# Kernel optimization log

Measured on AMD Instinct MI355X. Metric: run time of the kernel, lower is better.

Reference implementation:

```python
import jax, jax.numpy as jnp
import numpy as np

TWO_PI = 2.0 * 3.14159  # matches the torch source constant exactly
N_RINGS = 5
N_ORIENT = 8


def setup_inputs() -> dict:
    key = jax.random.key(0)
    k1, k2, k3 = jax.random.split(key, 3)
    B, N, CIN, COUT = 4, 32768, 32, 32
    features = jax.random.normal(k1, (B, N, CIN), dtype=jnp.float32)
    # radial in [0,1), angular in [0, 2*pi)
    coords01 = jax.random.uniform(k2, (B, N, 2), dtype=jnp.float32)
    geodesic_coords = coords01 * jnp.array([1.0, TWO_PI], dtype=jnp.float32)
    filters = jax.random.normal(k3, (N_RINGS, N_ORIENT, CIN, COUT), dtype=jnp.float32) * 0.01
    bias = jnp.zeros((COUT,), dtype=jnp.float32)
    return {"features": features, "geodesic_coords": geodesic_coords,
            "filters": filters, "bias": bias}


def reference(features, geodesic_coords, filters, bias):
    radial = geodesic_coords[:, :, 0]
    angular = geodesic_coords[:, :, 1]
    # torch .long() truncates toward zero; values are non-negative so astype matches
    ring_idx = jnp.clip((radial * N_RINGS).astype(jnp.int32), 0, N_RINGS - 1)
    orient_idx = jnp.clip((angular * N_ORIENT / TWO_PI).astype(jnp.int32), 0, N_ORIENT - 1)
    # gather per-point filter matrix: (B, N, Cin, Cout)
    W = filters[ring_idx, orient_idx]
    out = jnp.einsum('bnc,bncd->bnd', features, W) + bias
    return out
```

## Files before the change

kernel.cpp:

```cpp
#include <hip/hip_runtime.h>


#define NBINS 40
#define THREADS 1024
#define PTS_BLK 512

typedef __attribute__((ext_vector_type(8))) short bf16x8;
typedef __attribute__((ext_vector_type(4))) float f32x4;

__device__ __forceinline__ unsigned short f2bf(float x) {
    unsigned u = __float_as_uint(x);
    u += 0x7FFFu + ((u >> 16) & 1u);
    return (unsigned short)(u >> 16);
}

__device__ __forceinline__ int bin_of(float2 rc) {
    const float TWO_PI_F = (float)(2.0 * 3.14159);
    int ri = (int)(rc.x * 5.0f);
    ri = min(max(ri, 0), 4);
    int oi = (int)((rc.y * 8.0f) / TWO_PI_F);
    oi = min(max(oi, 0), 7);
    return ri * 8 + oi;
}

__global__ __launch_bounds__(THREADS, 4)
void k_fused(const float* __restrict__ feat, const float2* __restrict__ coords,
             const float* __restrict__ filt, const float* __restrict__ bias,
             float* __restrict__ out) {
    __shared__ __align__(16) unsigned short Wl[NBINS * 2 * 64 * 8];
    __shared__ int wlist[16][32];

    const int tid  = threadIdx.x;
    const int lane = tid & 63;
    const int wave = tid >> 6;
    const int l15  = lane & 15;
    const int kg   = lane >> 4;
    const int pbase = blockIdx.x * PTS_BLK + wave * 32;

    for (int it = tid; it < NBINS * 128; it += THREADS) {
        const int il = it & 15, ik = (it >> 4) & 3, in = (it >> 6) & 1, ib = it >> 7;
        const float* src = filt + ib * 1024 + ik * 256 + in * 16 + il;
        bf16x8 w;
        #pragma unroll
        for (int j = 0; j < 8; ++j) w[j] = (short)f2bf(src[j * 32]);
        *reinterpret_cast<bf16x8*>(&Wl[it * 8]) = w;
    }

    const int myb = bin_of(coords[pbase + (lane & 31)]);
    bf16x8 af[2];
    #pragma unroll
    for (int m = 0; m < 2; ++m) {
        const float* fp = feat + (size_t)(pbase + m * 16 + l15) * 32 + kg * 8;
        const float4 v0 = *reinterpret_cast<const float4*>(fp);
        const float4 v1 = *reinterpret_cast<const float4*>(fp + 4);
        bf16x8 a;
        a[0] = (short)f2bf(v0.x); a[1] = (short)f2bf(v0.y);
        a[2] = (short)f2bf(v0.z); a[3] = (short)f2bf(v0.w);
        a[4] = (short)f2bf(v1.x); a[5] = (short)f2bf(v1.y);
        a[6] = (short)f2bf(v1.z); a[7] = (short)f2bf(v1.w);
        af[m] = a;
    }
    const int bm0 = __shfl(myb, l15);
    const int bm1 = __shfl(myb, 16 + l15);

    int cnt = 0;
    unsigned long long rem = __ballot(1);
    while (rem) {
        const int src = (int)__ffsll((long long)rem) - 1;
        const int bb  = __shfl(myb, src);
        rem &= ~__ballot(myb == bb);
        if (lane == 0) wlist[wave][cnt] = bb;
        ++cnt;
    }

    __syncthreads();

    f32x4 acc[2][2];
    {
        const float bv0 = bias[l15];
        const float bv1 = bias[16 + l15];
        #pragma unroll
        for (int m = 0; m < 2; ++m) {
            acc[m][0] = (f32x4){bv0, bv0, bv0, bv0};
            acc[m][1] = (f32x4){bv1, bv1, bv1, bv1};
        }
    }

    int bb = wlist[wave][0];
    bf16x8 B0 = *reinterpret_cast<const bf16x8*>(&Wl[((bb * 2 + 0) * 64 + lane) * 8]);
    bf16x8 B1 = *reinterpret_cast<const bf16x8*>(&Wl[((bb * 2 + 1) * 64 + lane) * 8]);
    for (int i = 0; i < cnt; ++i) {
        const int nx  = (i + 1 < cnt) ? i + 1 : i;
        const int bbn = wlist[wave][nx];
        const bf16x8 N0 = *reinterpret_cast<const bf16x8*>(&Wl[((bbn * 2 + 0) * 64 + lane) * 8]);
        const bf16x8 N1 = *reinterpret_cast<const bf16x8*>(&Wl[((bbn * 2 + 1) * 64 + lane) * 8]);
        bf16x8 a0 = af[0]; if (bm0 != bb) a0 = (bf16x8)0;
        bf16x8 a1 = af[1]; if (bm1 != bb) a1 = (bf16x8)0;
        acc[0][0] = __builtin_amdgcn_mfma_f32_16x16x32_bf16(a0, B0, acc[0][0], 0, 0, 0);
        acc[0][1] = __builtin_amdgcn_mfma_f32_16x16x32_bf16(a0, B1, acc[0][1], 0, 0, 0);
        acc[1][0] = __builtin_amdgcn_mfma_f32_16x16x32_bf16(a1, B0, acc[1][0], 0, 0, 0);
        acc[1][1] = __builtin_amdgcn_mfma_f32_16x16x32_bf16(a1, B1, acc[1][1], 0, 0, 0);
        bb = bbn; B0 = N0; B1 = N1;
    }

    #pragma unroll
    for (int m = 0; m < 2; ++m)
        #pragma unroll
        for (int r = 0; r < 4; ++r) {
            const size_t o = (size_t)(pbase + m * 16 + kg * 4 + r) * 32;
            out[o + l15]      = acc[m][0][r];
            out[o + 16 + l15] = acc[m][1][r];
        }
}

extern "C" void kernel_launch(void* const* d_in, const int* in_sizes, int n_in,
                              void* d_out, int out_size, void* d_ws, size_t ws_size,
                              hipStream_t stream) {
    const float*  feat   = (const float*)d_in[0];
    const float2* coords = (const float2*)d_in[1];
    const float*  filt   = (const float*)d_in[2];
    const float*  bias   = (const float*)d_in[3];
    float* out = (float*)d_out;

    const int npts = in_sizes[0] / 32;
    k_fused<<<npts / PTS_BLK, THREADS, 0, stream>>>(feat, coords, filt, bias, out);
}
```

Before: 80.87 us.

## Sort block points by bin and load filter fragments directly from global

Each block now builds a histogram of its 512 points' bins in shared memory, computes prefix offsets, and ranks points so that each wave processes points grouped by filter bin. This cuts the number of distinct bins per wave and so the number of masked MFMA passes. The per-block conversion of all 40 filters into LDS is removed, and each wave instead gathers and converts its needed filter fragments straight from global memory with strided scalar loads. The cost is extra syncs and atomics, gathered feature and output rows that are no longer contiguous, and uncoalesced filter loads on the critical path.

```diff
diff --git a/kernel.cpp b/kernel.cpp
--- a/kernel.cpp
+++ b/kernel.cpp
@@ -27,7 +27,10 @@
 void k_fused(const float* __restrict__ feat, const float2* __restrict__ coords,
              const float* __restrict__ filt, const float* __restrict__ bias,
              float* __restrict__ out) {
-    __shared__ __align__(16) unsigned short Wl[NBINS * 2 * 64 * 8];
+    __shared__ int hist[NBINS];
+    __shared__ int offs[NBINS];
+    __shared__ int bins[PTS_BLK];
+    __shared__ int rank[PTS_BLK];
     __shared__ int wlist[16][32];
 
     const int tid  = threadIdx.x;
@@ -35,22 +38,40 @@
     const int wave = tid >> 6;
     const int l15  = lane & 15;
     const int kg   = lane >> 4;
-    const int pbase = blockIdx.x * PTS_BLK + wave * 32;
+    const int pbase = blockIdx.x * PTS_BLK;
 
-    for (int it = tid; it < NBINS * 128; it += THREADS) {
-        const int il = it & 15, ik = (it >> 4) & 3, in = (it >> 6) & 1, ib = it >> 7;
-        const float* src = filt + ib * 1024 + ik * 256 + in * 16 + il;
-        bf16x8 w;
+    if (tid < NBINS) hist[tid] = 0;
+    __syncthreads();
+    if (tid < PTS_BLK) {
+        const int b = bin_of(coords[pbase + tid]);
+        bins[tid] = b;
+        atomicAdd(&hist[b], 1);
+    }
+    __syncthreads();
+    if (wave == 0) {
+        int v = (lane < NBINS) ? hist[lane] : 0;
         #pragma unroll
-        for (int j = 0; j < 8; ++j) w[j] = (short)f2bf(src[j * 32]);
-        *reinterpret_cast<bf16x8*>(&Wl[it * 8]) = w;
+        for (int o = 1; o < 64; o <<= 1) { int t = __shfl_up(v, o); if (lane >= o) v += t; }
+        int e = __shfl_up(v, 1); if (lane == 0) e = 0;
+        if (lane < NBINS) offs[lane] = e;
     }
+    __syncthreads();
+    if (tid < PTS_BLK) {
+        const int r = atomicAdd(&offs[bins[tid]], 1);
+        rank[r] = tid;
+    }
+    __syncthreads();
 
-    const int myb = bin_of(coords[pbase + (lane & 31)]);
+    const int wbase = wave * 32;
+    const int myb = bins[rank[wbase + (lane & 31)]];
+
+    int lidx[2], bm[2];
     bf16x8 af[2];
     #pragma unroll
     for (int m = 0; m < 2; ++m) {
-        const float* fp = feat + (size_t)(pbase + m * 16 + l15) * 32 + kg * 8;
+        lidx[m] = rank[wbase + m * 16 + l15];
+        bm[m]   = bins[lidx[m]];
+        const float* fp = feat + (size_t)(pbase + lidx[m]) * 32 + kg * 8;
         const float4 v0 = *reinterpret_cast<const float4*>(fp);
         const float4 v1 = *reinterpret_cast<const float4*>(fp + 4);
         bf16x8 a;
@@ -60,8 +81,6 @@
         a[6] = (short)f2bf(v1.z); a[7] = (short)f2bf(v1.w);
         af[m] = a;
     }
-    const int bm0 = __shfl(myb, l15);
-    const int bm1 = __shfl(myb, 16 + l15);
 
     int cnt = 0;
     unsigned long long rem = __ballot(1);
@@ -72,8 +91,6 @@
         if (lane == 0) wlist[wave][cnt] = bb;
         ++cnt;
     }
-
-    __syncthreads();
 
     f32x4 acc[2][2];
     {
@@ -86,16 +103,27 @@
         }
     }
 
+    const float* bsrc = filt + kg * 256 + l15;
+#define LOAD_B(BB, O0, O1) {                                                  \
+        const float* s = bsrc + (BB) * 1024;                                  \
+        bf16x8 t0, t1;                                                        \
+        _Pragma("unroll")                                                     \
+        for (int j = 0; j < 8; ++j) {                                         \
+            t0[j] = (short)f2bf(s[j * 32]);                                   \
+            t1[j] = (short)f2bf(s[j * 32 + 16]);                              \
+        }                                                                     \
+        O0 = t0; O1 = t1;                                                     \
+    }
+
     int bb = wlist[wave][0];
-    bf16x8 B0 = *reinterpret_cast<const bf16x8*>(&Wl[((bb * 2 + 0) * 64 + lane) * 8]);
-    bf16x8 B1 = *reinterpret_cast<const bf16x8*>(&Wl[((bb * 2 + 1) * 64 + lane) * 8]);
+    bf16x8 B0, B1, N0, N1;
+    LOAD_B(bb, B0, B1)
     for (int i = 0; i < cnt; ++i) {
         const int nx  = (i + 1 < cnt) ? i + 1 : i;
         const int bbn = wlist[wave][nx];
-        const bf16x8 N0 = *reinterpret_cast<const bf16x8*>(&Wl[((bbn * 2 + 0) * 64 + lane) * 8]);
-        const bf16x8 N1 = *reinterpret_cast<const bf16x8*>(&Wl[((bbn * 2 + 1) * 64 + lane) * 8]);
-        bf16x8 a0 = af[0]; if (bm0 != bb) a0 = (bf16x8)0;
-        bf16x8 a1 = af[1]; if (bm1 != bb) a1 = (bf16x8)0;
+        LOAD_B(bbn, N0, N1)
+        bf16x8 a0 = af[0]; if (bm[0] != bb) a0 = (bf16x8)0;
+        bf16x8 a1 = af[1]; if (bm[1] != bb) a1 = (bf16x8)0;
         acc[0][0] = __builtin_amdgcn_mfma_f32_16x16x32_bf16(a0, B0, acc[0][0], 0, 0, 0);
         acc[0][1] = __builtin_amdgcn_mfma_f32_16x16x32_bf16(a0, B1, acc[0][1], 0, 0, 0);
         acc[1][0] = __builtin_amdgcn_mfma_f32_16x16x32_bf16(a1, B0, acc[1][0], 0, 0, 0);
@@ -107,7 +135,8 @@
     for (int m = 0; m < 2; ++m)
         #pragma unroll
         for (int r = 0; r < 4; ++r) {
-            const size_t o = (size_t)(pbase + m * 16 + kg * 4 + r) * 32;
+            const int row = rank[wbase + m * 16 + kg * 4 + r];
+            const size_t o = (size_t)(pbase + row) * 32;
             out[o + l15]      = acc[m][0][r];
             out[o + 16 + l15] = acc[m][1][r];
         }
```

New measurement: 80.70 us. Within noise of the previous version (-0.2%).
